# Kernel optimization log

Hardware: AMD Instinct MI355X
Metric: run time of the kernel (lower is better)

## Reference

```python
import jax, jax.numpy as jnp
import numpy as np

DIM = 1024
CTX_DIM = 1024
HEADS = 16
HEAD_DIM = DIM // HEADS


def setup_inputs() -> dict:
    key = jax.random.key(0)
    ks = jax.random.split(key, 6)
    B, N, M = 2, 2048, 2048
    s = 0.02
    return {
        "x": jax.random.normal(ks[0], (B, N, DIM), dtype=jnp.float32),
        "context": jax.random.normal(ks[1], (B, M, CTX_DIM), dtype=jnp.float32),
        "W_q": jax.random.normal(ks[2], (DIM, DIM), dtype=jnp.float32) * s,
        "W_kv": jax.random.normal(ks[3], (CTX_DIM * 2, CTX_DIM), dtype=jnp.float32) * s,
        "W_proj": jax.random.normal(ks[4], (DIM, DIM), dtype=jnp.float32) * s,
        "b_proj": jax.random.normal(ks[5], (DIM,), dtype=jnp.float32) * s,
    }


def reference(x, context, W_q, W_kv, W_proj, b_proj):
    B, N, C = x.shape
    M = context.shape[1]
    scale = HEAD_DIM ** (-0.5)
    # q projection: [B,N,H,D]
    q = (x @ W_q.T).reshape(B, N, HEADS, HEAD_DIM) * scale
    # context kv projection: [B,M,2,H,D]
    kv = (context @ W_kv.T).reshape(B, M, 2, HEADS, HEAD_DIM)
    k = kv[:, :, 0]  # [B,M,H,D]
    v = kv[:, :, 0]  # NOTE: source uses qkv_context[0] for BOTH k and v (faithful)
    attn = jnp.einsum("bnhd,bmhd->bhnm", q, k)
    attn = jax.nn.softmax(attn, axis=-1)
    out = jnp.einsum("bhnm,bmhd->bnhd", attn, v).reshape(B, N, C)
    return out @ W_proj.T + b_proj
```

## Files before the change

kernel.cpp:

```cpp
#include <hip/hip_runtime.h>
#include <hip/hip_bf16.h>


typedef __bf16 bf16x8 __attribute__((ext_vector_type(8)));
typedef float f32x4 __attribute__((ext_vector_type(4)));
typedef float f32x16 __attribute__((ext_vector_type(16)));

static constexpr int kDIM = 1024;
static constexpr float kLog2e = 1.4426950408889634f;

__device__ inline unsigned short f2bf(float f) {
    union { float f; unsigned int u; } v; v.f = f;
    return (unsigned short)((v.u + 0x7FFFu + ((v.u >> 16) & 1u)) >> 16);
}

__device__ inline unsigned int cvtpk2bf(float a, float b) {
    unsigned int r;
    asm("v_cvt_pk_bf16_f32 %0, %1, %2" : "=v"(r) : "v"(a), "v"(b));
    return r;
}

__device__ inline void gload_lds16(const unsigned short* g, unsigned short* l) {
    __builtin_amdgcn_global_load_lds(
        (const __attribute__((address_space(1))) unsigned int*)g,
        (__attribute__((address_space(3))) unsigned int*)l, 16, 0, 0);
}

__global__ __launch_bounds__(256) void cast_all(
    const float* __restrict__ x, const float* __restrict__ ctx,
    const float* __restrict__ wq, const float* __restrict__ wkv,
    const float* __restrict__ wp,
    unsigned short* __restrict__ xb, unsigned short* __restrict__ cb,
    unsigned short* __restrict__ wqb, unsigned short* __restrict__ wkb,
    unsigned short* __restrict__ wpb)
{
    int j = blockIdx.x * 256 + threadIdx.x;
    const float* s; unsigned short* d;
    if (j < 1048576)                      { s = x;   d = xb;  }
    else if ((j -= 1048576) < 1048576)    { s = ctx; d = cb;  }
    else if ((j -= 1048576) < 262144)     { s = wq;  d = wqb; }
    else if ((j -= 262144) < 262144)      { s = wkv; d = wkb; }
    else if ((j -= 262144) < 262144)      { s = wp;  d = wpb; }
    else return;
    float4 f = ((const float4*)s)[j];
    ushort4 o;
    o.x = f2bf(f.x); o.y = f2bf(f.y); o.z = f2bf(f.z); o.w = f2bf(f.w);
    ((ushort4*)d)[j] = o;
}

__global__ __launch_bounds__(512, 4) void gemm_qk(
    const unsigned short* __restrict__ xb, const unsigned short* __restrict__ cb,
    const unsigned short* __restrict__ Wq, const unsigned short* __restrict__ Wkv,
    unsigned short* __restrict__ Qb, unsigned short* __restrict__ Kb,
    unsigned short* __restrict__ Ktb, float qscale, int Mctx)
{
    __shared__ unsigned short As[128 * 64];
    __shared__ unsigned short Bs[128 * 64];

    const int lin  = blockIdx.x + 8 * blockIdx.y + 256 * blockIdx.z;
    const int orig = (lin & 7) * 64 + (lin >> 3);
    const int bxi  = orig & 7;
    const int byi  = (orig >> 3) & 31;
    const int z    = orig >> 8;

    const unsigned short* A  = z ? cb : xb;
    const unsigned short* Bw = z ? Wkv : Wq;
    unsigned short* Cb = z ? Kb : Qb;
    const float scale = z ? 1.0f : qscale;

    const int tid = threadIdx.x;
    const int wave = tid >> 6, lane = tid & 63;
    const int g = lane >> 4, c = lane & 15;
    const int wm = (wave >> 2) * 64, wn = (wave & 3) * 32;
    const int bm = byi * 128, bn = bxi * 128;

    const int srow = lane >> 3;
    const int scolsw = ((lane & 7) ^ (srow & 7)) * 8;
    const int x7 = c & 7;

    f32x4 acc[4][2];
    #pragma unroll
    for (int i = 0; i < 4; ++i)
        #pragma unroll
        for (int j = 0; j < 2; ++j)
            acc[i][j] = (f32x4){0.f, 0.f, 0.f, 0.f};

    for (int k0 = 0; k0 < kDIM; k0 += 64) {
        __syncthreads();
        #pragma unroll
        for (int t = 0; t < 2; ++t) {
            const int chunk = wave * 2 + t;
            gload_lds16(A + (size_t)(bm + chunk * 8 + srow) * kDIM + k0 + scolsw,
                        &As[chunk * 512]);
        }
        #pragma unroll
        for (int t = 0; t < 2; ++t) {
            const int chunk = wave * 2 + t;
            gload_lds16(Bw + (size_t)(bn + chunk * 8 + srow) * kDIM + k0 + scolsw,
                        &Bs[chunk * 512]);
        }
        __syncthreads();
        #pragma unroll
        for (int kc = 0; kc < 2; ++kc) {
            bf16x8 af[4], bfr[2];
            #pragma unroll
            for (int i = 0; i < 4; ++i)
                af[i] = *(const bf16x8*)&As[(wm + i * 16 + c) * 64 +
                                            ((kc * 4 + g) ^ x7) * 8];
            #pragma unroll
            for (int j = 0; j < 2; ++j)
                bfr[j] = *(const bf16x8*)&Bs[(wn + j * 16 + c) * 64 +
                                             ((kc * 4 + g) ^ x7) * 8];
            #pragma unroll
            for (int i = 0; i < 4; ++i)
                #pragma unroll
                for (int j = 0; j < 2; ++j)
                    acc[i][j] = __builtin_amdgcn_mfma_f32_16x16x32_bf16(
                        af[i], bfr[j], acc[i][j], 0, 0, 0);
        }
    }

    #pragma unroll
    for (int i = 0; i < 4; ++i) {
        #pragma unroll
        for (int j = 0; j < 2; ++j) {
            const int r0 = bm + wm + i * 16 + 4 * g;
            const int cc = bn + wn + j * 16 + c;
            float v0 = acc[i][j][0] * scale;
            float v1 = acc[i][j][1] * scale;
            float v2 = acc[i][j][2] * scale;
            float v3 = acc[i][j][3] * scale;
            Cb[(size_t)(r0 + 0) * kDIM + cc] = f2bf(v0);
            Cb[(size_t)(r0 + 1) * kDIM + cc] = f2bf(v1);
            Cb[(size_t)(r0 + 2) * kDIM + cc] = f2bf(v2);
            Cb[(size_t)(r0 + 3) * kDIM + cc] = f2bf(v3);
            if (z) {
                const int bb = r0 / Mctx, n0 = r0 % Mctx;
                const int hh = cc >> 6, d = cc & 63;
                ushort4 pk;
                pk.x = f2bf(v0); pk.y = f2bf(v1); pk.z = f2bf(v2); pk.w = f2bf(v3);
                *(ushort4*)&Ktb[((size_t)((bb * 16 + hh) * 64 + d)) * Mctx + n0] = pk;
            }
        }
    }
}

__global__ __launch_bounds__(256, 4) void gemm_proj(
    const unsigned short* __restrict__ Ab, const unsigned short* __restrict__ Wp,
    const float* __restrict__ bias, float* __restrict__ out)
{
    __shared__ unsigned short As[64 * 64];
    __shared__ unsigned short Bs[64 * 64];

    const int lin  = blockIdx.x + 16 * blockIdx.y;
    const int orig = (lin & 7) * 128 + (lin >> 3);
    const int bm = (orig >> 4) * 64, bn = (orig & 15) * 64;

    const int tid = threadIdx.x;
    const int wave = tid >> 6, lane = tid & 63;
    const int g = lane >> 4, c = lane & 15;
    const int wm = (wave & 1) * 32, wn = (wave >> 1) * 32;

    const int srow = lane >> 3;
    const int scolsw = ((lane & 7) ^ (srow & 7)) * 8;
    const int x7 = c & 7;

    f32x4 acc[2][2];
    #pragma unroll
    for (int i = 0; i < 2; ++i)
        #pragma unroll
        for (int j = 0; j < 2; ++j)
            acc[i][j] = (f32x4){0.f, 0.f, 0.f, 0.f};

    for (int k0 = 0; k0 < kDIM; k0 += 64) {
        __syncthreads();
        #pragma unroll
        for (int t = 0; t < 2; ++t) {
            const int chunk = wave * 2 + t;
            const int row = chunk * 8 + srow;
            gload_lds16(Ab + (size_t)(bm + row) * kDIM + k0 + scolsw, &As[chunk * 512]);
            gload_lds16(Wp + (size_t)(bn + row) * kDIM + k0 + scolsw, &Bs[chunk * 512]);
        }
        __syncthreads();
        #pragma unroll
        for (int kc = 0; kc < 2; ++kc) {
            bf16x8 af[2], bfr[2];
            #pragma unroll
            for (int i = 0; i < 2; ++i)
                af[i] = *(const bf16x8*)&As[(wm + i * 16 + c) * 64 +
                                            ((kc * 4 + g) ^ x7) * 8];
            #pragma unroll
            for (int j = 0; j < 2; ++j)
                bfr[j] = *(const bf16x8*)&Bs[(wn + j * 16 + c) * 64 +
                                             ((kc * 4 + g) ^ x7) * 8];
            #pragma unroll
            for (int i = 0; i < 2; ++i)
                #pragma unroll
                for (int j = 0; j < 2; ++j)
                    acc[i][j] = __builtin_amdgcn_mfma_f32_16x16x32_bf16(
                        af[i], bfr[j], acc[i][j], 0, 0, 0);
        }
    }

    #pragma unroll
    for (int i = 0; i < 2; ++i) {
        #pragma unroll
        for (int j = 0; j < 2; ++j) {
            const int r0 = bm + wm + i * 16 + 4 * g;
            const int cc = bn + wn + j * 16 + c;
            const float bv = bias[cc];
            #pragma unroll
            for (int ii = 0; ii < 4; ++ii)
                out[(size_t)(r0 + ii) * kDIM + cc] = acc[i][j][ii] + bv;
        }
    }
}

__global__ __launch_bounds__(512, 4) void attn_mfma_v9(
    const unsigned short* __restrict__ Q,
    const unsigned short* __restrict__ K,
    const unsigned short* __restrict__ Kt,
    unsigned short* __restrict__ O, int N, int M)
{
    __shared__ unsigned short smem[18432];

    const int lin  = blockIdx.x + 16 * (blockIdx.y + 16 * blockIdx.z);
    const int orig = (lin & 7) * 64 + (lin >> 3);
    const int q0 = (orig & 15) * 128;
    const int h  = (orig >> 4) & 15;
    const int b  = orig >> 8;

    const int tid = threadIdx.x;
    const int w = tid >> 6, lane = tid & 63;
    const int strip = w >> 1, kh = w & 1;
    const int ql = lane & 31, l5 = lane >> 5;

    const unsigned short* Qrow = Q + (size_t)(b * N + q0 + strip * 32 + ql) * kDIM + h * 64;
    const unsigned short* Kb = K + (size_t)b * M * kDIM + h * 64;
    const unsigned short* Ktb = Kt + (size_t)((b * 16 + h) * 64) * M;

    bf16x8 bq[4];
    #pragma unroll
    for (int kc = 0; kc < 4; ++kc)
        bq[kc] = *(const bf16x8*)(Qrow + kc * 16 + l5 * 8);

    f32x16 ot[2];
    #pragma unroll
    for (int dt = 0; dt < 2; ++dt)
        #pragma unroll
        for (int r = 0; r < 16; ++r) ot[dt][r] = 0.f;
    float lac = 0.f;

    const int srow = tid >> 3, scol = (tid & 7) * 8;
    const int NT = M / 64;

    uint4 rk  = *(const uint4*)(Kb  + (size_t)srow * kDIM + scol);
    uint4 rkt = *(const uint4*)(Ktb + (size_t)srow * M + scol);
    *(uint4*)&smem[srow * 72 + scol]        = rk;
    *(uint4*)&smem[4608 + srow * 72 + scol] = rkt;
    rk  = *(const uint4*)(Kb  + (size_t)(64 + srow) * kDIM + scol);
    rkt = *(const uint4*)(Ktb + (size_t)srow * M + 64 + scol);
    __syncthreads();

    for (int t = 0; t < NT; ++t) {
        const int cur = t & 1;
        const unsigned short* Ksc  = smem + cur * 9216;
        const unsigned short* Ktsc = smem + cur * 9216 + 4608;

        if (t + 1 < NT) {
            unsigned short* Ksn = smem + (cur ^ 1) * 9216;
            *(uint4*)&Ksn[srow * 72 + scol]        = rk;
            *(uint4*)&Ksn[4608 + srow * 72 + scol] = rkt;
        }
        if (t + 2 < NT) {
            rk  = *(const uint4*)(Kb  + (size_t)((t + 2) * 64 + srow) * kDIM + scol);
            rkt = *(const uint4*)(Ktb + (size_t)srow * M + (t + 2) * 64 + scol);
        }

        f32x16 st;
        #pragma unroll
        for (int r = 0; r < 16; ++r) st[r] = 0.f;
        __builtin_amdgcn_s_setprio(1);
        #pragma unroll
        for (int kc = 0; kc < 4; ++kc) {
            bf16x8 ak = *(const bf16x8*)&Ksc[(kh * 32 + ql) * 72 + kc * 16 + l5 * 8];
            st = __builtin_amdgcn_mfma_f32_32x32x16_bf16(ak, bq[kc], st, 0, 0, 0);
        }
        __builtin_amdgcn_s_setprio(0);

        float pr[16];
        #pragma unroll
        for (int r = 0; r < 16; ++r) {
            pr[r] = __builtin_amdgcn_exp2f(st[r]);
            lac += pr[r];
        }
        unsigned int dw[8];
        #pragma unroll
        for (int p = 0; p < 8; ++p) dw[p] = cvtpk2bf(pr[2 * p], pr[2 * p + 1]);

        auto s02 = __builtin_amdgcn_permlane32_swap(dw[0], dw[2], false, false);
        auto s13 = __builtin_amdgcn_permlane32_swap(dw[1], dw[3], false, false);
        auto s46 = __builtin_amdgcn_permlane32_swap(dw[4], dw[6], false, false);
        auto s57 = __builtin_amdgcn_permlane32_swap(dw[5], dw[7], false, false);
        union BP { unsigned int u[4]; bf16x8 v; };
        BP b0, b1;
        b0.u[0] = s02[0]; b0.u[1] = s13[0]; b0.u[2] = s02[1]; b0.u[3] = s13[1];
        b1.u[0] = s46[0]; b1.u[1] = s57[0]; b1.u[2] = s46[1]; b1.u[3] = s57[1];
        bf16x8 bp[2] = { b0.v, b1.v };

        __builtin_amdgcn_s_setprio(1);
        #pragma unroll
        for (int kc2 = 0; kc2 < 2; ++kc2) {
            #pragma unroll
            for (int dt = 0; dt < 2; ++dt) {
                bf16x8 av = *(const bf16x8*)&Ktsc[(dt * 32 + ql) * 72 + kh * 32 + kc2 * 16 + l5 * 8];
                ot[dt] = __builtin_amdgcn_mfma_f32_32x32x16_bf16(av, bp[kc2], ot[dt], 0, 0, 0);
            }
        }
        __builtin_amdgcn_s_setprio(0);

        __syncthreads();
    }

    float lw = lac + __shfl_xor(lac, 32);
    float* Om = (float*)smem;
    float* Lm = Om + 128 * 68;
    const int qi = strip * 32 + ql;

    if (kh == 1) {
        #pragma unroll
        for (int dt = 0; dt < 2; ++dt)
            #pragma unroll
            for (int rr = 0; rr < 4; ++rr)
                *(f32x4*)&Om[qi * 68 + dt * 32 + 8 * rr + 4 * l5] =
                    (f32x4){ot[dt][4 * rr], ot[dt][4 * rr + 1],
                            ot[dt][4 * rr + 2], ot[dt][4 * rr + 3]};
        if (l5 == 0) Lm[qi] = lw;
    }
    __syncthreads();
    if (kh == 0) {
        const float inv = 1.0f / (lw + Lm[qi]);
        unsigned short* Ob = O + (size_t)(b * N + q0 + qi) * kDIM + h * 64;
        #pragma unroll
        for (int dt = 0; dt < 2; ++dt)
            #pragma unroll
            for (int rr = 0; rr < 4; ++rr) {
                f32x4 pv = *(const f32x4*)&Om[qi * 68 + dt * 32 + 8 * rr + 4 * l5];
                ushort4 u;
                u.x = f2bf((ot[dt][4 * rr]     + pv[0]) * inv);
                u.y = f2bf((ot[dt][4 * rr + 1] + pv[1]) * inv);
                u.z = f2bf((ot[dt][4 * rr + 2] + pv[2]) * inv);
                u.w = f2bf((ot[dt][4 * rr + 3] + pv[3]) * inv);
                *(ushort4*)(Ob + dt * 32 + 8 * rr + 4 * l5) = u;
            }
    }
}

extern "C" void kernel_launch(void* const* d_in, const int* in_sizes, int n_in,
                              void* d_out, int out_size, void* d_ws, size_t ws_size,
                              hipStream_t stream)
{
    const float* x      = (const float*)d_in[0];
    const float* ctxp   = (const float*)d_in[1];
    const float* W_q    = (const float*)d_in[2];
    const float* W_kv   = (const float*)d_in[3];
    const float* W_proj = (const float*)d_in[4];
    const float* b_proj = (const float*)d_in[5];
    float* out = (float*)d_out;

    const int B = 2, N = 2048, M = 2048;
    const int BN = B * N;
    const int SQ = kDIM * kDIM;

    unsigned short* p = (unsigned short*)d_ws;
    unsigned short* xb  = p; p += (size_t)BN * kDIM;
    unsigned short* cb  = p; p += (size_t)BN * kDIM;
    unsigned short* wqb = p; p += SQ;
    unsigned short* wkb = p; p += SQ;
    unsigned short* wpb = p; p += SQ;
    unsigned short* Qb  = p; p += (size_t)BN * kDIM;
    unsigned short* Kb  = p; p += (size_t)BN * kDIM;
    unsigned short* Ktb = p; p += (size_t)BN * kDIM;
    unsigned short* Ab  = xb;

    hipLaunchKernelGGL(cast_all, dim3(11264), dim3(256), 0, stream,
                       x, ctxp, W_q, W_kv, W_proj, xb, cb, wqb, wkb, wpb);
    hipLaunchKernelGGL(gemm_qk, dim3(kDIM / 128, BN / 128, 2), dim3(512), 0, stream,
                       xb, cb, wqb, wkb, Qb, Kb, Ktb, 0.125f * kLog2e, M);
    hipLaunchKernelGGL(attn_mfma_v9, dim3(N / 128, 16, B), dim3(512), 0, stream,
                       Qb, Kb, Ktb, Ab, N, M);
    hipLaunchKernelGGL(gemm_proj, dim3(kDIM / 64, BN / 64), dim3(256), 0, stream,
                       Ab, wpb, b_proj, out);
}
```

Before: 178.0 us.

## Software-pipeline PV MFMAs across tiles and enlarge proj GEMM M-tile

The attention loop now defers each tile's P·V MFMAs to the next iteration. They are issued right after the next tile's QK MFMAs, so matrix work overlaps the exp/convert/permlane softmax stage. The V fragments are loaded from LDS into registers before the barrier, and the last tile's MFMAs are drained after the loop, with an added sync before LDS is reused. Separately, the projection GEMM moves to 128x64 tiles with 512 threads, which halves the number of blocks and reuses each W tile across more rows. This raises register pressure and could lower occupancy.

```diff
diff --git a/kernel.cpp b/kernel.cpp
--- a/kernel.cpp
+++ b/kernel.cpp
@@ -145,21 +145,21 @@
     }
 }
 
-__global__ __launch_bounds__(256, 4) void gemm_proj(
+__global__ __launch_bounds__(512, 4) void gemm_proj(
     const unsigned short* __restrict__ Ab, const unsigned short* __restrict__ Wp,
     const float* __restrict__ bias, float* __restrict__ out)
 {
-    __shared__ unsigned short As[64 * 64];
+    __shared__ unsigned short As[128 * 64];
     __shared__ unsigned short Bs[64 * 64];
 
     const int lin  = blockIdx.x + 16 * blockIdx.y;
-    const int orig = (lin & 7) * 128 + (lin >> 3);
-    const int bm = (orig >> 4) * 64, bn = (orig & 15) * 64;
+    const int orig = (lin & 7) * 64 + (lin >> 3);
+    const int bm = (orig >> 4) * 128, bn = (orig & 15) * 64;
 
     const int tid = threadIdx.x;
     const int wave = tid >> 6, lane = tid & 63;
     const int g = lane >> 4, c = lane & 15;
-    const int wm = (wave & 1) * 32, wn = (wave >> 1) * 32;
+    const int wm = (wave >> 1) * 32, wn = (wave & 1) * 32;
 
     const int srow = lane >> 3;
     const int scolsw = ((lane & 7) ^ (srow & 7)) * 8;
@@ -177,10 +177,11 @@
         #pragma unroll
         for (int t = 0; t < 2; ++t) {
             const int chunk = wave * 2 + t;
-            const int row = chunk * 8 + srow;
-            gload_lds16(Ab + (size_t)(bm + row) * kDIM + k0 + scolsw, &As[chunk * 512]);
-            gload_lds16(Wp + (size_t)(bn + row) * kDIM + k0 + scolsw, &Bs[chunk * 512]);
-        }
+            gload_lds16(Ab + (size_t)(bm + chunk * 8 + srow) * kDIM + k0 + scolsw,
+                        &As[chunk * 512]);
+        }
+        gload_lds16(Wp + (size_t)(bn + wave * 8 + srow) * kDIM + k0 + scolsw,
+                    &Bs[wave * 512]);
         __syncthreads();
         #pragma unroll
         for (int kc = 0; kc < 2; ++kc) {
@@ -216,7 +217,7 @@
     }
 }
 
-__global__ __launch_bounds__(512, 4) void attn_mfma_v9(
+__global__ __launch_bounds__(512, 4) void attn_mfma_v10(
     const unsigned short* __restrict__ Q,
     const unsigned short* __restrict__ K,
     const unsigned short* __restrict__ Kt,
@@ -262,6 +263,10 @@
     rkt = *(const uint4*)(Ktb + (size_t)srow * M + 64 + scol);
     __syncthreads();
 
+    bf16x8 bpP0, bpP1;
+    bf16x8 avP0, avP1, avP2, avP3;
+    union BP { unsigned int u[4]; bf16x8 v; };
+
     for (int t = 0; t < NT; ++t) {
         const int cur = t & 1;
         const unsigned short* Ksc  = smem + cur * 9216;
@@ -286,6 +291,12 @@
             bf16x8 ak = *(const bf16x8*)&Ksc[(kh * 32 + ql) * 72 + kc * 16 + l5 * 8];
             st = __builtin_amdgcn_mfma_f32_32x32x16_bf16(ak, bq[kc], st, 0, 0, 0);
         }
+        if (t > 0) {
+            ot[0] = __builtin_amdgcn_mfma_f32_32x32x16_bf16(avP0, bpP0, ot[0], 0, 0, 0);
+            ot[1] = __builtin_amdgcn_mfma_f32_32x32x16_bf16(avP1, bpP0, ot[1], 0, 0, 0);
+            ot[0] = __builtin_amdgcn_mfma_f32_32x32x16_bf16(avP2, bpP1, ot[0], 0, 0, 0);
+            ot[1] = __builtin_amdgcn_mfma_f32_32x32x16_bf16(avP3, bpP1, ot[1], 0, 0, 0);
+        }
         __builtin_amdgcn_s_setprio(0);
 
         float pr[16];
@@ -297,36 +308,34 @@
         unsigned int dw[8];
         #pragma unroll
         for (int p = 0; p < 8; ++p) dw[p] = cvtpk2bf(pr[2 * p], pr[2 * p + 1]);
-
         auto s02 = __builtin_amdgcn_permlane32_swap(dw[0], dw[2], false, false);
         auto s13 = __builtin_amdgcn_permlane32_swap(dw[1], dw[3], false, false);
         auto s46 = __builtin_amdgcn_permlane32_swap(dw[4], dw[6], false, false);
         auto s57 = __builtin_amdgcn_permlane32_swap(dw[5], dw[7], false, false);
-        union BP { unsigned int u[4]; bf16x8 v; };
         BP b0, b1;
         b0.u[0] = s02[0]; b0.u[1] = s13[0]; b0.u[2] = s02[1]; b0.u[3] = s13[1];
         b1.u[0] = s46[0]; b1.u[1] = s57[0]; b1.u[2] = s46[1]; b1.u[3] = s57[1];
-        bf16x8 bp[2] = { b0.v, b1.v };
-
-        __builtin_amdgcn_s_setprio(1);
-        #pragma unroll
-        for (int kc2 = 0; kc2 < 2; ++kc2) {
-            #pragma unroll
-            for (int dt = 0; dt < 2; ++dt) {
-                bf16x8 av = *(const bf16x8*)&Ktsc[(dt * 32 + ql) * 72 + kh * 32 + kc2 * 16 + l5 * 8];
-                ot[dt] = __builtin_amdgcn_mfma_f32_32x32x16_bf16(av, bp[kc2], ot[dt], 0, 0, 0);
-            }
-        }
-        __builtin_amdgcn_s_setprio(0);
+        bpP0 = b0.v; bpP1 = b1.v;
+
+        avP0 = *(const bf16x8*)&Ktsc[(0 * 32 + ql) * 72 + kh * 32 + 0 * 16 + l5 * 8];
+        avP1 = *(const bf16x8*)&Ktsc[(1 * 32 + ql) * 72 + kh * 32 + 0 * 16 + l5 * 8];
+        avP2 = *(const bf16x8*)&Ktsc[(0 * 32 + ql) * 72 + kh * 32 + 1 * 16 + l5 * 8];
+        avP3 = *(const bf16x8*)&Ktsc[(1 * 32 + ql) * 72 + kh * 32 + 1 * 16 + l5 * 8];
 
         __syncthreads();
     }
+
+    ot[0] = __builtin_amdgcn_mfma_f32_32x32x16_bf16(avP0, bpP0, ot[0], 0, 0, 0);
+    ot[1] = __builtin_amdgcn_mfma_f32_32x32x16_bf16(avP1, bpP0, ot[1], 0, 0, 0);
+    ot[0] = __builtin_amdgcn_mfma_f32_32x32x16_bf16(avP2, bpP1, ot[0], 0, 0, 0);
+    ot[1] = __builtin_amdgcn_mfma_f32_32x32x16_bf16(avP3, bpP1, ot[1], 0, 0, 0);
 
     float lw = lac + __shfl_xor(lac, 32);
     float* Om = (float*)smem;
     float* Lm = Om + 128 * 68;
     const int qi = strip * 32 + ql;
 
+    __syncthreads();
     if (kh == 1) {
         #pragma unroll
         for (int dt = 0; dt < 2; ++dt)
@@ -387,8 +396,8 @@
                        x, ctxp, W_q, W_kv, W_proj, xb, cb, wqb, wkb, wpb);
     hipLaunchKernelGGL(gemm_qk, dim3(kDIM / 128, BN / 128, 2), dim3(512), 0, stream,
                        xb, cb, wqb, wkb, Qb, Kb, Ktb, 0.125f * kLog2e, M);
-    hipLaunchKernelGGL(attn_mfma_v9, dim3(N / 128, 16, B), dim3(512), 0, stream,
+    hipLaunchKernelGGL(attn_mfma_v10, dim3(N / 128, 16, B), dim3(512), 0, stream,
                        Qb, Kb, Ktb, Ab, N, M);
-    hipLaunchKernelGGL(gemm_proj, dim3(kDIM / 64, BN / 64), dim3(256), 0, stream,
+    hipLaunchKernelGGL(gemm_proj, dim3(kDIM / 64, BN / 128), dim3(512), 0, stream,
                        Ab, wpb, b_proj, out);
 }
```

New measurement: 177.7 us. Within noise of the previous version (-0.2%).
